# Kernel optimization log

Hardware: AMD Instinct MI355X
Metric: run time of the kernel (lower is better)

The kernel has to match this reference:

```python
import jax, jax.numpy as jnp
import numpy as np

B, N, FIELD_DIM, OUT_DIM = 65536, 128, 16, 64


def setup_inputs() -> dict:
    key = jax.random.key(0)
    k1, k2 = jax.random.split(key)
    x = jax.random.normal(k1, (B, N), dtype=jnp.float32)
    # learned FFM kernel: (n_features, field_dim, output_dim), uniform init like keras 'uniform'
    kernel = jax.random.uniform(k2, (N, FIELD_DIM, OUT_DIM), dtype=jnp.float32, minval=-0.05, maxval=0.05)
    # feature i belongs to field i % FIELD_DIM (the field_dict of the layer)
    field_dict = jnp.arange(N, dtype=jnp.int32) % FIELD_DIM
    return {"x": x, "kernel": kernel, "field_dict": field_dict}


def reference(x, kernel, field_dict):
    # Original math: out_b = sum_{i<j} <kernel[i, fd[j]], kernel[j, fd[i]]> * x[b,i] * x[b,j]
    n = kernel.shape[0]
    # A[i, j, k] = kernel[i, field_dict[j], k]  -> [N, N, OUT_DIM] (small: 128*128*64)
    A = kernel[:, field_dict, :]
    # S[i, j] = <kernel[i, fd[j]], kernel[j, fd[i]]>
    S = jnp.einsum('ijk,jik->ij', A, A)
    mask = jnp.triu(jnp.ones((n, n), dtype=S.dtype), k=1)  # i < j only
    Sm = S * mask
    # bilinear form per sample: sum_{i<j} S_ij x_i x_j
    return jnp.einsum('bi,ij,bj->b', x, Sm, x)
```

## Files before the change

### kernel.cpp

```cpp
#include <hip/hip_runtime.h>

#define NB 65536
#define NN 128
#define FDIM 16
#define ODIM 64

typedef __attribute__((ext_vector_type(8))) short s16x8;
typedef __attribute__((ext_vector_type(4))) float f32x4;

__device__ __forceinline__ unsigned short f2bf(float f) {
    unsigned u = __builtin_bit_cast(unsigned, f);
    u += 0x7FFFu + ((u >> 16) & 1u);
    return (unsigned short)(u >> 16);
}
__device__ __forceinline__ float bf2f(unsigned short h) {
    unsigned u = ((unsigned)h) << 16;
    return __builtin_bit_cast(float, u);
}

__global__ void prep_w(const float* __restrict__ kern, const int* __restrict__ fd,
                       unsigned short* __restrict__ wfrag) {
    int i = blockIdx.x;
    int j = threadIdx.x;
    int fi = fd[i], fj = fd[j];
    const float4* a = (const float4*)(kern + (i * FDIM + fj) * ODIM);
    const float4* b = (const float4*)(kern + (j * FDIM + fi) * ODIM);
    float s = 0.f;
#pragma unroll
    for (int k = 0; k < ODIM / 4; ++k) {
        float4 av = a[k], bv = b[k];
        s += av.x * bv.x + av.y * bv.y + av.z * bv.z + av.w * bv.w;
    }
    float w = (i == j) ? 0.f : 0.5f * s;
    int kt = i >> 5, kc = (i >> 3) & 3, e = i & 7;
    int nt = j >> 4;
    int lane = kc * 16 + (j & 15);
    wfrag[((nt * 4 + kt) * 64 + lane) * 8 + e] = f2bf(w);
}

__global__ __launch_bounds__(256) void qform(const float* __restrict__ x,
                                             const unsigned short* __restrict__ wfrag,
                                             float* __restrict__ out) {
    __shared__ __align__(16) unsigned short wlds[8 * 4 * 64 * 8];
    __shared__ __align__(16) unsigned short xlds[4][16][136];

    int tid = threadIdx.x;
    {
        const uint4* src = (const uint4*)wfrag;
        uint4* dst = (uint4*)wlds;
#pragma unroll
        for (int t = 0; t < 8; ++t) dst[t * 256 + tid] = src[t * 256 + tid];
    }

    int wave = tid >> 6, lane = tid & 63;
    int row = lane & 15;
    int kc = lane >> 4;
    int tile = blockIdx.x * 4 + wave;
    const float* xp = x + (tile * 16 + row) * NN;

    s16x8 ah[4], al[4];
#pragma unroll
    for (int kt = 0; kt < 4; ++kt) {
        const float4* p4 = (const float4*)(xp + kt * 32 + kc * 8);
        float4 v0 = p4[0], v1 = p4[1];
        float vs[8] = {v0.x, v0.y, v0.z, v0.w, v1.x, v1.y, v1.z, v1.w};
        unsigned short hb[8];
#pragma unroll
        for (int e = 0; e < 8; ++e) {
            hb[e] = f2bf(vs[e]);
            ah[kt][e] = (short)hb[e];
            float lo = vs[e] - bf2f(hb[e]);
            al[kt][e] = (short)f2bf(lo);
        }
        s16x8 hv;
#pragma unroll
        for (int e = 0; e < 8; ++e) hv[e] = (short)hb[e];
        *(s16x8*)&xlds[wave][row][kt * 32 + kc * 8] = hv;
    }
    __syncthreads();

    f32x4 acc[8];
#pragma unroll
    for (int nt = 0; nt < 8; ++nt) {
        f32x4 c = {0.f, 0.f, 0.f, 0.f};
#pragma unroll
        for (int kt = 0; kt < 4; ++kt) {
            s16x8 bf = *(const s16x8*)&wlds[((nt * 4 + kt) * 64 + lane) * 8];
            c = __builtin_amdgcn_mfma_f32_16x16x32_bf16(ah[kt], bf, c, 0, 0, 0);
            c = __builtin_amdgcn_mfma_f32_16x16x32_bf16(al[kt], bf, c, 0, 0, 0);
        }
        acc[nt] = c;
    }

    int rg = lane >> 4, cl = lane & 15;
    float p0 = 0.f, p1 = 0.f, p2 = 0.f, p3 = 0.f;
#pragma unroll
    for (int nt = 0; nt < 8; ++nt) {
        int c0 = nt * 16 + cl;
        p0 += acc[nt][0] * bf2f(xlds[wave][rg * 4 + 0][c0]);
        p1 += acc[nt][1] * bf2f(xlds[wave][rg * 4 + 1][c0]);
        p2 += acc[nt][2] * bf2f(xlds[wave][rg * 4 + 2][c0]);
        p3 += acc[nt][3] * bf2f(xlds[wave][rg * 4 + 3][c0]);
    }
#pragma unroll
    for (int m = 1; m <= 8; m <<= 1) {
        p0 += __shfl_xor(p0, m, 64);
        p1 += __shfl_xor(p1, m, 64);
        p2 += __shfl_xor(p2, m, 64);
        p3 += __shfl_xor(p3, m, 64);
    }
    if (cl == 0) {
        int ob = tile * 16 + rg * 4;
        out[ob + 0] = p0;
        out[ob + 1] = p1;
        out[ob + 2] = p2;
        out[ob + 3] = p3;
    }
}

extern "C" void kernel_launch(void* const* d_in, const int* in_sizes, int n_in,
                              void* d_out, int out_size, void* d_ws, size_t ws_size,
                              hipStream_t stream) {
    const float* x = (const float*)d_in[0];
    const float* kern = (const float*)d_in[1];
    const int* fd = (const int*)d_in[2];
    float* out = (float*)d_out;
    unsigned short* wfrag = (unsigned short*)d_ws;

    prep_w<<<dim3(NN), dim3(NN), 0, stream>>>(kern, fd, wfrag);
    qform<<<dim3(NB / 64), dim3(256), 0, stream>>>(x, wfrag, out);
}
```

Before: 18.64 us.

## Use direct global-to-LDS weight copy and 8-wave blocks in qform

The weight-fragment staging now uses the gfx950 global_load_lds builtin, which writes global memory straight into LDS without passing through registers. Blocks grow from 4 to 8 waves, so each 32 KB weight copy is shared by twice as many 16-row tiles and the grid halves to 512 blocks. The low-part bf16 split of x now truncates instead of rounding, which saves ALU work at a small precision cost. prep_w also splits its dot product across four accumulators to shorten the dependency chain.

```diff
diff --git a/kernel.cpp b/kernel.cpp
--- a/kernel.cpp
+++ b/kernel.cpp
@@ -8,7 +8,10 @@
 typedef __attribute__((ext_vector_type(8))) short s16x8;
 typedef __attribute__((ext_vector_type(4))) float f32x4;
 
-__device__ __forceinline__ unsigned short f2bf(float f) {
+typedef __attribute__((address_space(3))) void lds_void_t;
+typedef const __attribute__((address_space(1))) void gbl_void_t;
+
+__device__ __forceinline__ unsigned short f2bf_rne(float f) {
     unsigned u = __builtin_bit_cast(unsigned, f);
     u += 0x7FFFu + ((u >> 16) & 1u);
     return (unsigned short)(u >> 16);
@@ -25,37 +28,42 @@
     int fi = fd[i], fj = fd[j];
     const float4* a = (const float4*)(kern + (i * FDIM + fj) * ODIM);
     const float4* b = (const float4*)(kern + (j * FDIM + fi) * ODIM);
-    float s = 0.f;
+    float s[4] = {0.f, 0.f, 0.f, 0.f};
 #pragma unroll
     for (int k = 0; k < ODIM / 4; ++k) {
         float4 av = a[k], bv = b[k];
-        s += av.x * bv.x + av.y * bv.y + av.z * bv.z + av.w * bv.w;
+        s[k & 3] += av.x * bv.x + av.y * bv.y + av.z * bv.z + av.w * bv.w;
     }
-    float w = (i == j) ? 0.f : 0.5f * s;
+    float w = (i == j) ? 0.f : 0.5f * (s[0] + s[1] + s[2] + s[3]);
     int kt = i >> 5, kc = (i >> 3) & 3, e = i & 7;
     int nt = j >> 4;
     int lane = kc * 16 + (j & 15);
-    wfrag[((nt * 4 + kt) * 64 + lane) * 8 + e] = f2bf(w);
+    wfrag[((nt * 4 + kt) * 64 + lane) * 8 + e] = f2bf_rne(w);
 }
 
-__global__ __launch_bounds__(256) void qform(const float* __restrict__ x,
-                                             const unsigned short* __restrict__ wfrag,
-                                             float* __restrict__ out) {
+__global__ __launch_bounds__(512, 4) void qform(const float* __restrict__ x,
+                                                const unsigned short* __restrict__ wfrag,
+                                                float* __restrict__ out) {
     __shared__ __align__(16) unsigned short wlds[8 * 4 * 64 * 8];
-    __shared__ __align__(16) unsigned short xlds[4][16][136];
+    __shared__ __align__(16) unsigned short xlds[8][16][136];
 
     int tid = threadIdx.x;
+    int wave = tid >> 6, lane = tid & 63;
+
     {
-        const uint4* src = (const uint4*)wfrag;
-        uint4* dst = (uint4*)wlds;
+        const char* gsrc = (const char*)wfrag;
+        char* ldst = (char*)wlds;
 #pragma unroll
-        for (int t = 0; t < 8; ++t) dst[t * 256 + tid] = src[t * 256 + tid];
+        for (int t = 0; t < 4; ++t) {
+            int off = (wave * 4 + t) * 1024 + lane * 16;
+            __builtin_amdgcn_global_load_lds((gbl_void_t*)(gsrc + off),
+                                             (lds_void_t*)(ldst + off), 16, 0, 0);
+        }
     }
 
-    int wave = tid >> 6, lane = tid & 63;
     int row = lane & 15;
     int kc = lane >> 4;
-    int tile = blockIdx.x * 4 + wave;
+    int tile = blockIdx.x * 8 + wave;
     const float* xp = x + (tile * 16 + row) * NN;
 
     s16x8 ah[4], al[4];
@@ -64,17 +72,15 @@
         const float4* p4 = (const float4*)(xp + kt * 32 + kc * 8);
         float4 v0 = p4[0], v1 = p4[1];
         float vs[8] = {v0.x, v0.y, v0.z, v0.w, v1.x, v1.y, v1.z, v1.w};
-        unsigned short hb[8];
+        s16x8 hv;
 #pragma unroll
         for (int e = 0; e < 8; ++e) {
-            hb[e] = f2bf(vs[e]);
-            ah[kt][e] = (short)hb[e];
-            float lo = vs[e] - bf2f(hb[e]);
-            al[kt][e] = (short)f2bf(lo);
+            unsigned short hb = f2bf_rne(vs[e]);
+            hv[e] = (short)hb;
+            ah[kt][e] = (short)hb;
+            float lo = vs[e] - bf2f(hb);
+            al[kt][e] = (short)(unsigned short)(__builtin_bit_cast(unsigned, lo) >> 16);
         }
-        s16x8 hv;
-#pragma unroll
-        for (int e = 0; e < 8; ++e) hv[e] = (short)hb[e];
         *(s16x8*)&xlds[wave][row][kt * 32 + kc * 8] = hv;
     }
     __syncthreads();
@@ -128,5 +134,5 @@
     unsigned short* wfrag = (unsigned short*)d_ws;
 
     prep_w<<<dim3(NN), dim3(NN), 0, stream>>>(kern, fd, wfrag);
-    qform<<<dim3(NB / 64), dim3(256), 0, stream>>>(x, wfrag, out);
+    qform<<<dim3(512), dim3(512), 0, stream>>>(x, wfrag, out);
 }
```

After: 18.05 us. -3.2%, faster.
